# Kernel optimization log

Hardware: AMD Instinct MI355X
Metric: run time of the kernel (lower is better)

The kernel has to match this reference:

```python
import jax, jax.numpy as jnp
import numpy as np

B, N, EDGES = 16, 50000, 1600000
CLAMP_MIN, CLAMP_MAX = -10.0, 10.0
EPS = 1e-6


def setup_inputs() -> dict:
    key = jax.random.key(0)
    ks = jax.random.split(key, 8)
    return {
        "chem_influence": jax.random.normal(ks[0], (B, N), dtype=jnp.float32),
        "E": jax.random.normal(ks[1], (B, N), dtype=jnp.float32),
        "o_pre": jax.random.uniform(ks[2], (B, N), dtype=jnp.float32),
        "w": jax.random.normal(ks[3], (EDGES,), dtype=jnp.float32),
        "threshold": jax.random.uniform(ks[4], (N,), dtype=jnp.float32),
        "decay": jax.random.uniform(ks[5], (N,), dtype=jnp.float32),
        "src": jax.random.randint(ks[6], (EDGES,), 0, N, dtype=jnp.int32),
        "dst": jax.random.randint(ks[7], (EDGES,), 0, N, dtype=jnp.int32),
    }


def reference(chem_influence, E, o_pre, w, threshold, decay, src, dst):
    # Gap-junction currents: gather, sign-compare, weighted scatter-add.
    Oj = o_pre[:, src]                      # (B, EDGES) presynaptic outputs
    En = E[:, dst]                          # (B, EDGES) postsynaptic internal states
    sgn = jnp.where(Oj >= En, 1.0, -1.0)
    contrib = Oj * w * sgn                  # (B, EDGES)
    gj_sum = jnp.zeros_like(chem_influence).at[:, dst].add(contrib)  # (B, N)

    # Neuron dynamics (eqs 10, 11).
    S = jnp.clip(E + chem_influence + gj_sum, CLAMP_MIN, CLAMP_MAX)
    gt = S > threshold                      # broadcast (N,) over (B, N)
    mask = (~gt) & (jnp.abs(S - E) <= EPS)
    new_o = jax.nn.relu(S - threshold)
    new_e = jnp.where(gt, new_o, jnp.where(mask, E - decay, S))
    return (new_o, new_e)
```

## Files before the change

kernel.cpp:

```cpp
#include <hip/hip_runtime.h>

#define BATCH 16
#define NNODES 50000
#define NEDGES 1600000
#define BN (BATCH * NNODES)
#define CLAMP_LO -10.0f
#define CLAMP_HI 10.0f
#define EPS_V 1e-6f

#define NBINS 782
#define BSZ 64
#define CAPE 2560
#define K1B 250
#define EPB 6400
#define E4PB 1600
#define NPT 200

__global__ __launch_bounds__(256) void prep_scatter(
    const float* __restrict__ o_pre, const float* __restrict__ E,
    const int* __restrict__ src, const int* __restrict__ dst,
    const float* __restrict__ w,
    float* __restrict__ o_t, float* __restrict__ E_t,
    int* __restrict__ cnt,
    uint2* __restrict__ binned) {
    __shared__ int lh[NBINS];
    __shared__ int cur[NBINS];
    const int tid = threadIdx.x, bid = blockIdx.x;

    for (int i = tid; i < NBINS; i += 256) lh[i] = 0;

    if (tid < NPT) {
        int t = bid * NPT + tid;
        float v[BATCH], u[BATCH];
#pragma unroll
        for (int b = 0; b < BATCH; ++b) {
            v[b] = o_pre[b * NNODES + t];
            u[b] = E[b * NNODES + t];
        }
        float4* op = (float4*)(o_t + (size_t)t * BATCH);
        float4* ep = (float4*)(E_t + (size_t)t * BATCH);
#pragma unroll
        for (int k = 0; k < 4; ++k) {
            op[k] = make_float4(v[4 * k], v[4 * k + 1], v[4 * k + 2], v[4 * k + 3]);
            ep[k] = make_float4(u[4 * k], u[4 * k + 1], u[4 * k + 2], u[4 * k + 3]);
        }
    }
    __syncthreads();

    const int4* dst4 = (const int4*)dst;
    const int i40 = bid * E4PB;
#pragma unroll
    for (int j = 0; j < 7; ++j) {
        int idx = j * 256 + tid;
        if (idx < E4PB) {
            int4 d4 = dst4[i40 + idx];
            atomicAdd(&lh[d4.x >> 6], 1);
            atomicAdd(&lh[d4.y >> 6], 1);
            atomicAdd(&lh[d4.z >> 6], 1);
            atomicAdd(&lh[d4.w >> 6], 1);
        }
    }
    __syncthreads();

    for (int i = tid; i < NBINS; i += 256) {
        int c = lh[i];
        cur[i] = i * CAPE + (c ? atomicAdd(&cnt[i], c) : 0);
    }
    __syncthreads();

    const int4*   src4 = (const int4*)src;
    const float4* w4   = (const float4*)w;
#pragma unroll
    for (int j = 0; j < 7; ++j) {
        int idx = j * 256 + tid;
        if (idx < E4PB) {
            int4 d4 = dst4[i40 + idx];
            int4 s4 = src4[i40 + idx];
            float4 ww = w4[i40 + idx];
            int dd[4] = {d4.x, d4.y, d4.z, d4.w};
            int ss[4] = {s4.x, s4.y, s4.z, s4.w};
            float wv[4] = {ww.x, ww.y, ww.z, ww.w};
#pragma unroll
            for (int m = 0; m < 4; ++m) {
                int d = dd[m];
                int bin = d >> 6;
                int pos = atomicAdd(&cur[bin], 1);
                if (pos < (bin + 1) * CAPE)
                    binned[pos] = make_uint2(
                        (unsigned)ss[m] | ((unsigned)(d & 63) << 16),
                        __float_as_uint(wv[m]));
            }
        }
    }
}

__global__ __launch_bounds__(256) void bin_gather2(
    const float* __restrict__ o_t, const float* __restrict__ E_t,
    const float* __restrict__ chem, const float* __restrict__ threshold,
    const float* __restrict__ decay, const int* __restrict__ cnt,
    const uint2* __restrict__ binned,
    float* __restrict__ out_o, float* __restrict__ out_e) {
    __shared__ int   cnt_l[BSZ];
    __shared__ int   offs[BSZ + 1];
    __shared__ int   sc[BSZ];
    __shared__ uint2 eb[CAPE];

    const int k = blockIdx.x, tid = threadIdx.x;
    const int node0 = k * BSZ;
    const int nn = (NNODES - node0 < BSZ) ? (NNODES - node0) : BSZ;
    const int s0 = k * CAPE;
    int c = cnt[k];
    if (c > CAPE) c = CAPE;
    const int s1 = s0 + c;

    if (tid < BSZ) cnt_l[tid] = 0;
    __syncthreads();
    for (int i = s0 + tid; i < s1; i += 256)
        atomicAdd(&cnt_l[(binned[i].x >> 16) & 63], 1);
    __syncthreads();

    if (tid < BSZ) sc[tid] = cnt_l[tid];
    __syncthreads();
    for (int o = 1; o < BSZ; o <<= 1) {
        int v = (tid >= o && tid < BSZ) ? sc[tid - o] : 0;
        __syncthreads();
        if (tid < BSZ) sc[tid] += v;
        __syncthreads();
    }
    if (tid < BSZ) {
        int ex = sc[tid] - cnt_l[tid];
        offs[tid] = ex;
        cnt_l[tid] = ex;
    }
    if (tid == 0) offs[BSZ] = c;
    __syncthreads();

    for (int i = s0 + tid; i < s1; i += 256) {
        uint2 p = binned[i];
        int pos = atomicAdd(&cnt_l[(p.x >> 16) & 63], 1);
        if (pos < CAPE) eb[pos] = p;
    }
    __syncthreads();

    if (tid < nn * 4) {
        int n = tid >> 2;
        int q = (tid & 3) * 4;
        int gn = node0 + n;
        int e0 = offs[n], e1 = offs[n + 1];
        float4 en = *(const float4*)(E_t + (size_t)gn * BATCH + q);
        float4 acc = make_float4(0.f, 0.f, 0.f, 0.f);
        for (int i = e0; i < e1; ++i) {
            uint2 p = eb[i];
            float wv = __uint_as_float(p.y);
            int s = (int)(p.x & 0xFFFFu);
            float4 oj = *(const float4*)(o_t + (size_t)s * BATCH + q);
            acc.x += (oj.x >= en.x) ? oj.x * wv : -oj.x * wv;
            acc.y += (oj.y >= en.y) ? oj.y * wv : -oj.y * wv;
            acc.z += (oj.z >= en.z) ? oj.z * wv : -oj.z * wv;
            acc.w += (oj.w >= en.w) ? oj.w * wv : -oj.w * wv;
        }
        float th = threshold[gn];
        float dc = decay[gn];
        float ev[4] = {en.x, en.y, en.z, en.w};
        float av[4] = {acc.x, acc.y, acc.z, acc.w};
#pragma unroll
        for (int j = 0; j < 4; ++j) {
            int b = q + j;
            float e = ev[j];
            float S = e + chem[b * NNODES + gn] + av[j];
            S = fminf(fmaxf(S, CLAMP_LO), CLAMP_HI);
            float no = fmaxf(S - th, 0.0f);
            float ne;
            if (S > th) ne = no;
            else if (fabsf(S - e) <= EPS_V) ne = e - dc;
            else ne = S;
            out_o[b * NNODES + gn] = no;
            out_e[b * NNODES + gn] = ne;
        }
    }
}

__global__ void edge_scatter_dev(const float* __restrict__ o_pre, const float* __restrict__ E,
                                 const float* __restrict__ w, const int* __restrict__ src,
                                 const int* __restrict__ dst, float* __restrict__ gj) {
    int e = blockIdx.x * blockDim.x + threadIdx.x;
    if (e >= NEDGES) return;
    int s = src[e];
    int d = dst[e];
    float wv = w[e];
#pragma unroll
    for (int b = 0; b < BATCH; ++b) {
        float oj = o_pre[b * NNODES + s];
        float en = E[b * NNODES + d];
        atomicAdd(&gj[b * NNODES + d], (oj >= en) ? oj * wv : -oj * wv);
    }
}

__global__ void finalize_dev(const float* __restrict__ chem, const float* __restrict__ E,
                             const float* __restrict__ threshold, const float* __restrict__ decay,
                             float* __restrict__ out_o, float* __restrict__ out_e_gj) {
    int i = blockIdx.x * blockDim.x + threadIdx.x;
    if (i >= BN) return;
    int n = i % NNODES;
    float e = E[i];
    float S = e + chem[i] + out_e_gj[i];
    S = fminf(fmaxf(S, CLAMP_LO), CLAMP_HI);
    float th = threshold[n];
    float no = fmaxf(S - th, 0.0f);
    float ne;
    if (S > th) ne = no;
    else if (fabsf(S - e) <= EPS_V) ne = e - decay[n];
    else ne = S;
    out_o[i] = no;
    out_e_gj[i] = ne;
}

extern "C" void kernel_launch(void* const* d_in, const int* in_sizes, int n_in,
                              void* d_out, int out_size, void* d_ws, size_t ws_size,
                              hipStream_t stream) {
    const float* chem      = (const float*)d_in[0];
    const float* E         = (const float*)d_in[1];
    const float* o_pre     = (const float*)d_in[2];
    const float* w         = (const float*)d_in[3];
    const float* threshold = (const float*)d_in[4];
    const float* decay     = (const float*)d_in[5];
    const int*   src       = (const int*)d_in[6];
    const int*   dst       = (const int*)d_in[7];

    float* out_o = (float*)d_out;
    float* out_e = (float*)d_out + BN;

    const size_t OT_OFF  = 0;
    const size_t ET_OFF  = 3200000;
    const size_t BIN_OFF = 6400000;
    const size_t CNT_OFF = 22415360;
    const size_t need    = CNT_OFF + (size_t)NBINS * sizeof(int);

    if (ws_size >= need) {
        char* ws = (char*)d_ws;
        float* o_t    = (float*)(ws + OT_OFF);
        float* E_t    = (float*)(ws + ET_OFF);
        uint2* binned = (uint2*)(ws + BIN_OFF);
        int*   cnt    = (int*)(ws + CNT_OFF);

        hipMemsetAsync(cnt, 0, (size_t)NBINS * sizeof(int), stream);
        prep_scatter<<<K1B, 256, 0, stream>>>(o_pre, E, src, dst, w,
                                              o_t, E_t, cnt, binned);
        bin_gather2<<<NBINS, 256, 0, stream>>>(o_t, E_t, chem, threshold, decay,
                                               cnt, binned, out_o, out_e);
    } else {
        hipMemsetAsync(out_e, 0, (size_t)BN * sizeof(float), stream);
        edge_scatter_dev<<<(NEDGES + 255) / 256, 256, 0, stream>>>(o_pre, E, w, src, dst, out_e);
        finalize_dev<<<(BN + 255) / 256, 256, 0, stream>>>(chem, E, threshold, decay, out_o, out_e);
    }
}
```

Before: 140.6 us.

## Replace global-atomic bin reservation with per-slice local sort and histogram table

Each of the first kernel's blocks now sorts its own edge slice by destination bin into a private region of the workspace and writes a prefix-sum histogram row. Global atomics on the bin counters and the memset that reset them are gone. The gather kernel has one thread per slice read that slice's segment for its bin, using the histogram rows. This trades contended global atomics and scattered writes for serial per-thread reads of short, uncoalesced segments in the gather kernel.

```diff
diff --git a/kernel.cpp b/kernel.cpp
--- a/kernel.cpp
+++ b/kernel.cpp
@@ -12,19 +12,21 @@
 #define BSZ 64
 #define CAPE 2560
 #define K1B 250
-#define EPB 6400
-#define E4PB 1600
+#define EPS 6400
+#define E4PS 1600
 #define NPT 200
-
-__global__ __launch_bounds__(256) void prep_scatter(
+#define HROW 784
+
+__global__ __launch_bounds__(256) void slice_sort(
     const float* __restrict__ o_pre, const float* __restrict__ E,
     const int* __restrict__ src, const int* __restrict__ dst,
     const float* __restrict__ w,
     float* __restrict__ o_t, float* __restrict__ E_t,
-    int* __restrict__ cnt,
+    int* __restrict__ hist,
     uint2* __restrict__ binned) {
     __shared__ int lh[NBINS];
     __shared__ int cur[NBINS];
+    __shared__ int sm[256];
     const int tid = threadIdx.x, bid = blockIdx.x;
 
     for (int i = tid; i < NBINS; i += 256) lh[i] = 0;
@@ -48,11 +50,11 @@
     __syncthreads();
 
     const int4* dst4 = (const int4*)dst;
-    const int i40 = bid * E4PB;
+    const int i40 = bid * E4PS;
 #pragma unroll
     for (int j = 0; j < 7; ++j) {
         int idx = j * 256 + tid;
-        if (idx < E4PB) {
+        if (idx < E4PS) {
             int4 d4 = dst4[i40 + idx];
             atomicAdd(&lh[d4.x >> 6], 1);
             atomicAdd(&lh[d4.y >> 6], 1);
@@ -62,18 +64,43 @@
     }
     __syncthreads();
 
-    for (int i = tid; i < NBINS; i += 256) {
-        int c = lh[i];
-        cur[i] = i * CAPE + (c ? atomicAdd(&cnt[i], c) : 0);
+    {
+        int base = tid * 4;
+        int v[4], psum = 0;
+#pragma unroll
+        for (int j = 0; j < 4; ++j) {
+            int idx = base + j;
+            v[j] = (idx < NBINS) ? lh[idx] : 0;
+            psum += v[j];
+        }
+        sm[tid] = psum;
+        __syncthreads();
+        for (int off = 1; off < 256; off <<= 1) {
+            int a = (tid >= off) ? sm[tid - off] : 0;
+            __syncthreads();
+            sm[tid] += a;
+            __syncthreads();
+        }
+        int run = (tid > 0) ? sm[tid - 1] : 0;
+#pragma unroll
+        for (int j = 0; j < 4; ++j) {
+            int idx = base + j;
+            if (idx < NBINS + 1) {
+                hist[(size_t)bid * HROW + idx] = run;
+                if (idx < NBINS) cur[idx] = run;
+            }
+            if (idx < NBINS) run += v[j];
+        }
     }
     __syncthreads();
 
     const int4*   src4 = (const int4*)src;
     const float4* w4   = (const float4*)w;
+    uint2* out = binned + (size_t)bid * EPS;
 #pragma unroll
     for (int j = 0; j < 7; ++j) {
         int idx = j * 256 + tid;
-        if (idx < E4PB) {
+        if (idx < E4PS) {
             int4 d4 = dst4[i40 + idx];
             int4 s4 = src4[i40 + idx];
             float4 ww = w4[i40 + idx];
@@ -83,21 +110,19 @@
 #pragma unroll
             for (int m = 0; m < 4; ++m) {
                 int d = dd[m];
-                int bin = d >> 6;
-                int pos = atomicAdd(&cur[bin], 1);
-                if (pos < (bin + 1) * CAPE)
-                    binned[pos] = make_uint2(
-                        (unsigned)ss[m] | ((unsigned)(d & 63) << 16),
-                        __float_as_uint(wv[m]));
+                int pos = atomicAdd(&cur[d >> 6], 1);
+                out[pos] = make_uint2(
+                    (unsigned)ss[m] | ((unsigned)(d & 63) << 16),
+                    __float_as_uint(wv[m]));
             }
         }
     }
 }
 
-__global__ __launch_bounds__(256) void bin_gather2(
+__global__ __launch_bounds__(256) void bin_gather3(
     const float* __restrict__ o_t, const float* __restrict__ E_t,
     const float* __restrict__ chem, const float* __restrict__ threshold,
-    const float* __restrict__ decay, const int* __restrict__ cnt,
+    const float* __restrict__ decay, const int* __restrict__ hist,
     const uint2* __restrict__ binned,
     float* __restrict__ out_o, float* __restrict__ out_e) {
     __shared__ int   cnt_l[BSZ];
@@ -108,15 +133,19 @@
     const int k = blockIdx.x, tid = threadIdx.x;
     const int node0 = k * BSZ;
     const int nn = (NNODES - node0 < BSZ) ? (NNODES - node0) : BSZ;
-    const int s0 = k * CAPE;
-    int c = cnt[k];
-    if (c > CAPE) c = CAPE;
-    const int s1 = s0 + c;
+
+    int st = 0, c = 0;
+    if (tid < K1B) {
+        st = hist[(size_t)tid * HROW + k];
+        int en = hist[(size_t)tid * HROW + k + 1];
+        c = en - st;
+    }
+    const uint2* sb = binned + (size_t)tid * EPS + st;
 
     if (tid < BSZ) cnt_l[tid] = 0;
     __syncthreads();
-    for (int i = s0 + tid; i < s1; i += 256)
-        atomicAdd(&cnt_l[(binned[i].x >> 16) & 63], 1);
+    for (int j = 0; j < c; ++j)
+        atomicAdd(&cnt_l[(sb[j].x >> 16) & 63], 1);
     __syncthreads();
 
     if (tid < BSZ) sc[tid] = cnt_l[tid];
@@ -132,11 +161,11 @@
         offs[tid] = ex;
         cnt_l[tid] = ex;
     }
-    if (tid == 0) offs[BSZ] = c;
-    __syncthreads();
-
-    for (int i = s0 + tid; i < s1; i += 256) {
-        uint2 p = binned[i];
+    if (tid == 0) offs[BSZ] = sc[BSZ - 1];
+    __syncthreads();
+
+    for (int j = 0; j < c; ++j) {
+        uint2 p = sb[j];
         int pos = atomicAdd(&cnt_l[(p.x >> 16) & 63], 1);
         if (pos < CAPE) eb[pos] = p;
     }
@@ -147,6 +176,7 @@
         int q = (tid & 3) * 4;
         int gn = node0 + n;
         int e0 = offs[n], e1 = offs[n + 1];
+        if (e1 > CAPE) e1 = CAPE;
         float4 en = *(const float4*)(E_t + (size_t)gn * BATCH + q);
         float4 acc = make_float4(0.f, 0.f, 0.f, 0.f);
         for (int i = e0; i < e1; ++i) {
@@ -233,21 +263,20 @@
     const size_t OT_OFF  = 0;
     const size_t ET_OFF  = 3200000;
     const size_t BIN_OFF = 6400000;
-    const size_t CNT_OFF = 22415360;
-    const size_t need    = CNT_OFF + (size_t)NBINS * sizeof(int);
+    const size_t H_OFF   = 19200000;
+    const size_t need    = H_OFF + (size_t)K1B * HROW * sizeof(int);
 
     if (ws_size >= need) {
         char* ws = (char*)d_ws;
         float* o_t    = (float*)(ws + OT_OFF);
         float* E_t    = (float*)(ws + ET_OFF);
         uint2* binned = (uint2*)(ws + BIN_OFF);
-        int*   cnt    = (int*)(ws + CNT_OFF);
-
-        hipMemsetAsync(cnt, 0, (size_t)NBINS * sizeof(int), stream);
-        prep_scatter<<<K1B, 256, 0, stream>>>(o_pre, E, src, dst, w,
-                                              o_t, E_t, cnt, binned);
-        bin_gather2<<<NBINS, 256, 0, stream>>>(o_t, E_t, chem, threshold, decay,
-                                               cnt, binned, out_o, out_e);
+        int*   hist   = (int*)(ws + H_OFF);
+
+        slice_sort<<<K1B, 256, 0, stream>>>(o_pre, E, src, dst, w,
+                                            o_t, E_t, hist, binned);
+        bin_gather3<<<NBINS, 256, 0, stream>>>(o_t, E_t, chem, threshold, decay,
+                                               hist, binned, out_o, out_e);
     } else {
         hipMemsetAsync(out_e, 0, (size_t)BN * sizeof(float), stream);
         edge_scatter_dev<<<(NEDGES + 255) / 256, 256, 0, stream>>>(o_pre, E, w, src, dst, out_e);
```

Result: slower. 145.0 us (+3.1%).
